# Kernel optimization log

Measured on AMD Instinct MI355X. Metric: run time of the kernel, lower is better.

Reference implementation:

```python
import jax, jax.numpy as jnp
import numpy as np

BITS = 4
N_PACK = 8          # 32-bit words / 4-bit values
GROUPSIZE = 128
MASK = (1 << BITS) - 1


def dequantize(qweight, qzeros, scales):
    """GPTQ/optimum-format int4 dequant.
    qweight: [in/8, out] int32, little-endian nibbles along packed (input) dim.
    qzeros:  [groups, out/8] int32, little-endian nibbles along packed (output) dim.
    scales:  [groups, out] float.
    Returns W: [in, out] float.
    """
    shifts = (jnp.arange(N_PACK, dtype=jnp.int32) * BITS)
    kpack, out_f = qweight.shape
    groups = scales.shape[0]
    # unpack weight nibbles -> [in, out]
    w_int = (qweight[:, None, :] >> shifts[None, :, None]) & MASK        # [in/8, 8, out]
    w_int = w_int.reshape(kpack * N_PACK, out_f)                          # [in, out]
    # unpack zero-point nibbles -> [groups, out]; optimum format adds 1 back
    zp = (qzeros[:, :, None] >> shifts[None, None, :]) & MASK             # [groups, out/8, 8]
    zp = zp.reshape(groups, out_f) + 1                                    # [groups, out]
    # group-wise dequant: (w - zp) * scale
    w_g = w_int.reshape(groups, GROUPSIZE, out_f).astype(scales.dtype)    # [G, gs, out]
    W = (w_g - zp[:, None, :].astype(scales.dtype)) * scales[:, None, :]
    return W.reshape(kpack * N_PACK, out_f)


def setup_inputs() -> dict:
    key = jax.random.key(0)
    k1, k2, k3, k4, k5 = jax.random.split(key, 5)
    in_f, out_f, groups = 4096, 11008, 4096 // GROUPSIZE
    tokens = 4096
    x = jax.random.normal(k1, (tokens, in_f), dtype=jnp.float32)
    qweight = jax.random.randint(k2, (in_f // N_PACK, out_f), 0, 2147483647, dtype=jnp.int32)
    qzeros = jax.random.randint(k3, (groups, out_f // N_PACK), 0, 2147483647, dtype=jnp.int32)
    scales = jax.random.uniform(k4, (groups, out_f), dtype=jnp.float32) * 0.01 + 0.001
    bias = jax.random.normal(k5, (out_f,), dtype=jnp.float32)
    return {"x": x, "qweight": qweight, "qzeros": qzeros, "scales": scales, "bias": bias}


def reference(x, qweight, qzeros, scales, bias):
    W = dequantize(qweight, qzeros, scales)   # [in, out]
    return x @ W + bias                        # F.linear(x, W.T, bias)
```

## Files before the change

### kernel.cpp

```cpp
#include <hip/hip_runtime.h>
#include <stdint.h>

typedef _Float16 h2 __attribute__((ext_vector_type(2)));
typedef _Float16 h8 __attribute__((ext_vector_type(8)));
typedef float f32x4 __attribute__((ext_vector_type(4)));

__device__ __forceinline__ uint32_t pk_cvt(float a, float b) {
  return __builtin_bit_cast(uint32_t, __builtin_amdgcn_cvt_pkrtz(a, b));
}

__device__ __forceinline__ uint32_t dq(uint32_t t, h2 z2, h2 s2) {
  h2 v = __builtin_bit_cast(h2, t);
  h2 w = (v - z2) * s2;
  return __builtin_bit_cast(uint32_t, w);
}

__device__ __forceinline__ uint32_t dq_lin(uint32_t u, h2 z2, h2 s2) {
  uint32_t t = (u & 0xFu) | ((u & 0xF0u) << 12) | 0x64006400u;
  return dq(t, z2, s2);
}

typedef __attribute__((address_space(1))) const uint32_t* gas_ptr;
typedef __attribute__((address_space(3))) uint32_t* las_ptr;
__device__ __forceinline__ void gll16(const _Float16* g, _Float16* l) {
  __builtin_amdgcn_global_load_lds((gas_ptr)g, (las_ptr)l, 16, 0, 0);
}

#define WAITVM(n) asm volatile("s_waitcnt vmcnt(" #n ")" ::: "memory")
#define MEMFENCE  asm volatile("" ::: "memory")

__global__ __launch_bounds__(256) void cvt_x_kernel(const float* __restrict__ x,
                                                    _Float16* __restrict__ xh,
                                                    size_t n) {
  size_t i = ((size_t)blockIdx.x * 256 + threadIdx.x) * 8;
  if (i >= n) return;
  float4 a = *(const float4*)(x + i);
  float4 b = *(const float4*)(x + i + 4);
  uint4 v = make_uint4(pk_cvt(a.x, a.y), pk_cvt(a.z, a.w),
                       pk_cvt(b.x, b.y), pk_cvt(b.z, b.w));
  *(uint4*)(xh + i) = v;
}

__global__ __launch_bounds__(256) void dequant_w_kernel(
    const uint32_t* __restrict__ qweight, const uint32_t* __restrict__ qzeros,
    const float* __restrict__ scales, _Float16* __restrict__ wt, int N, int K) {
  __shared__ uint32_t qw[8][64];
  const int t = threadIdx.x;
  const int n0 = blockIdx.x * 64;
  const int kp0 = blockIdx.y * 8;

  {
    int r = t >> 6, c = t & 63;
    qw[r][c]     = qweight[(size_t)(kp0 + r) * N + n0 + c];
    qw[r + 4][c] = qweight[(size_t)(kp0 + r + 4) * N + n0 + c];
  }
  __syncthreads();

  const int nl = t >> 2;
  const int kpl = (t & 3) * 2;
  const int n = n0 + nl;
  const int g = kp0 >> 4;
  uint32_t qz = qzeros[(size_t)g * (N >> 3) + (n >> 3)];
  int zp = (qz >> ((n & 7) * 4)) & 15;
  float sc = scales[(size_t)g * N + n];
  _Float16 hz = (_Float16)(float)(1024 + zp + 1);
  _Float16 hs = (_Float16)sc;
  h2 z2 = {hz, hz};
  h2 s2 = {hs, hs};

#pragma unroll
  for (int w = 0; w < 2; ++w) {
    uint32_t word = qw[kpl + w][nl];
    uint4 v = make_uint4(dq_lin(word, z2, s2), dq_lin(word >> 8, z2, s2),
                         dq_lin(word >> 16, z2, s2), dq_lin(word >> 24, z2, s2));
    *(uint4*)(wt + (size_t)n * K + (size_t)(kp0 + kpl + w) * 8) = v;
  }
}

__global__ __launch_bounds__(512, 2) void gemm_f16_256(
    const _Float16* __restrict__ A, const _Float16* __restrict__ B,
    const float* __restrict__ bias, float* __restrict__ out,
    int M, int N, int K) {
  __shared__ _Float16 As[4][256 * 32];
  __shared__ _Float16 Bs[4][256 * 32];

  const int gx = gridDim.x, gy = gridDim.y;
  const int nwg = gx * gy;
  const int lin = blockIdx.y * gx + blockIdx.x;
  const int xcd = lin & 7, idx = lin >> 3;
  const int q8 = nwg >> 3, r8 = nwg & 7;
  const int wg = (xcd < r8 ? xcd * (q8 + 1) : r8 * (q8 + 1) + (xcd - r8) * q8) + idx;
  const int bn0 = (wg % gx) * 256;
  const int bm0 = (wg / gx) * 256;

  const int tid = threadIdx.x;
  const int lane = tid & 63;
  const int wave = tid >> 6;
  const int wm = wave >> 2;
  const int wn = wave & 3;

  f32x4 acc[8][4];
#pragma unroll
  for (int i = 0; i < 8; ++i)
#pragma unroll
    for (int j = 0; j < 4; ++j) acc[i][j] = (f32x4)0.f;

  const int srow = lane >> 2;
  const int sslot = (lane & 3) ^ ((lane >> 3) & 3);
  const _Float16* pSa0 = A + (size_t)(bm0 + 32 * wave + srow) * K + sslot * 8;
  const _Float16* pSa1 = pSa0 + (size_t)16 * K;
  const _Float16* pSb0 = B + (size_t)(bn0 + 32 * wave + srow) * K + sslot * 8;
  const _Float16* pSb1 = pSb0 + (size_t)16 * K;
  const int dst_off = wave * 1024;

  const int fslot = ((lane >> 4) ^ ((lane >> 1) & 3)) * 8;
  const int aoff = (wm * 128 + (lane & 15)) * 32 + fslot;
  const int boff = (wn * 64 + (lane & 15)) * 32 + fslot;

  const int nt = K >> 5;

#pragma unroll
  for (int u = 0; u < 3; ++u) {
    if (u < nt) {
      const size_t ko = (size_t)u * 32;
      _Float16* da = As[u & 3] + dst_off;
      _Float16* db = Bs[u & 3] + dst_off;
      gll16(pSa0 + ko, da);
      gll16(pSa1 + ko, da + 512);
      gll16(pSb0 + ko, db);
      gll16(pSb1 + ko, db + 512);
    }
  }
  if (nt >= 3)      WAITVM(8);
  else if (nt == 2) WAITVM(4);
  else              WAITVM(0);
  __builtin_amdgcn_s_barrier();
  MEMFENCE;

  for (int t = 0; t < nt; ++t) {
    const int buf = t & 3;
    const _Float16* Ab = As[buf] + aoff;
    const _Float16* Bb = Bs[buf] + boff;
    const int ts = t + 3;
    const bool do_stage = ts < nt;
    const size_t ko = (size_t)ts * 32;
    _Float16* da = As[ts & 3] + dst_off;
    _Float16* db = Bs[ts & 3] + dst_off;

    h8 af[4], bf[4];
#pragma unroll
    for (int r = 0; r < 4; ++r) {
      af[r] = *(const h8*)(Ab + r * 512);
      bf[r] = *(const h8*)(Bb + r * 512);
    }
    if (do_stage) {
      gll16(pSa0 + ko, da);
      gll16(pSa1 + ko, da + 512);
    }
    __builtin_amdgcn_s_barrier();
    asm volatile("s_waitcnt lgkmcnt(0)" ::: "memory");
    __builtin_amdgcn_sched_barrier(0);
    __builtin_amdgcn_s_setprio(1);
#pragma unroll
    for (int r = 0; r < 4; ++r)
#pragma unroll
      for (int j = 0; j < 4; ++j)
        acc[r][j] = __builtin_amdgcn_mfma_f32_16x16x32_f16(af[r], bf[j],
                                                           acc[r][j], 0, 0, 0);
    __builtin_amdgcn_s_setprio(0);
    __builtin_amdgcn_s_barrier();
    MEMFENCE;

#pragma unroll
    for (int r = 0; r < 4; ++r) af[r] = *(const h8*)(Ab + (4 + r) * 512);
    if (do_stage) {
      gll16(pSb0 + ko, db);
      gll16(pSb1 + ko, db + 512);
    }
    if (do_stage)            WAITVM(8);
    else if (ts == nt)       WAITVM(4);
    else if (t + 2 == nt)    WAITVM(0);
    __builtin_amdgcn_s_barrier();
    asm volatile("s_waitcnt lgkmcnt(0)" ::: "memory");
    __builtin_amdgcn_sched_barrier(0);
    __builtin_amdgcn_s_setprio(1);
#pragma unroll
    for (int r = 0; r < 4; ++r)
#pragma unroll
      for (int j = 0; j < 4; ++j)
        acc[4 + r][j] = __builtin_amdgcn_mfma_f32_16x16x32_f16(af[r], bf[j],
                                                               acc[4 + r][j],
                                                               0, 0, 0);
    __builtin_amdgcn_s_setprio(0);
    __builtin_amdgcn_s_barrier();
    MEMFENCE;
  }

  const int r0 = bm0 + wm * 128 + ((lane >> 4) << 2);
  const int c0 = bn0 + wn * 64 + (lane & 15);
#pragma unroll
  for (int j = 0; j < 4; ++j) {
    const int c = c0 + j * 16;
    const float bv = bias[c];
#pragma unroll
    for (int i = 0; i < 8; ++i) {
#pragma unroll
      for (int rr = 0; rr < 4; ++rr)
        out[(size_t)(r0 + i * 16 + rr) * N + c] = acc[i][j][rr] + bv;
    }
  }
}

__global__ __launch_bounds__(256) void gemm_f16_kernel(
    const _Float16* __restrict__ A,
    const _Float16* __restrict__ B,
    const float* __restrict__ bias, float* __restrict__ out,
    int M, int N, int K) {
  __shared__ _Float16 As[128 * 32];
  __shared__ _Float16 Bs[128 * 32];

  const int tid = threadIdx.x;
  const int lane = tid & 63;
  const int wave = tid >> 6;
  const int wm = wave & 1;
  const int wn = wave >> 1;
  const int bn0 = blockIdx.x * 128;
  const int bm0 = blockIdx.y * 128;

  f32x4 acc[4][4];
#pragma unroll
  for (int i = 0; i < 4; ++i)
#pragma unroll
    for (int j = 0; j < 4; ++j) acc[i][j] = (f32x4)0.f;

  const int srow = wave * 16 + (lane >> 2);
  const int skoff = (lane & 3) * 8;
  const _Float16* Ag0 = A + (size_t)(bm0 + srow) * K + skoff;
  const _Float16* Ag1 = A + (size_t)(bm0 + 64 + srow) * K + skoff;
  const _Float16* Bg0 = B + (size_t)(bn0 + srow) * K + skoff;
  const _Float16* Bg1 = B + (size_t)(bn0 + 64 + srow) * K + skoff;
  _Float16* Al0 = As + (wave * 16) * 32;
  _Float16* Al1 = As + (64 + wave * 16) * 32;
  _Float16* Bl0 = Bs + (wave * 16) * 32;
  _Float16* Bl1 = Bs + (64 + wave * 16) * 32;

  const _Float16* Af = As + (wm * 64 + (lane & 15)) * 32 + (lane >> 4) * 8;
  const _Float16* Bf = Bs + (wn * 64 + (lane & 15)) * 32 + (lane >> 4) * 8;

  for (int k0 = 0; k0 < K; k0 += 32) {
    gll16(Ag0 + k0, Al0);
    gll16(Ag1 + k0, Al1);
    gll16(Bg0 + k0, Bl0);
    gll16(Bg1 + k0, Bl1);
    __syncthreads();

    h8 af[4], bf[4];
#pragma unroll
    for (int i = 0; i < 4; ++i) {
      af[i] = *(const h8*)(Af + i * 16 * 32);
      bf[i] = *(const h8*)(Bf + i * 16 * 32);
    }
#pragma unroll
    for (int i = 0; i < 4; ++i)
#pragma unroll
      for (int j = 0; j < 4; ++j)
        acc[i][j] = __builtin_amdgcn_mfma_f32_16x16x32_f16(af[i], bf[j],
                                                           acc[i][j], 0, 0, 0);
    __syncthreads();
  }

  const int r0 = bm0 + wm * 64 + (lane >> 4) * 4;
  const int c0 = bn0 + wn * 64 + (lane & 15);
#pragma unroll
  for (int j = 0; j < 4; ++j) {
    const int c = c0 + j * 16;
    const float bv = bias[c];
#pragma unroll
    for (int i = 0; i < 4; ++i) {
#pragma unroll
      for (int rr = 0; rr < 4; ++rr) {
        out[(size_t)(r0 + i * 16 + rr) * N + c] = acc[i][j][rr] + bv;
      }
    }
  }
}

#define LDK 40
__global__ __launch_bounds__(256) void gptq_gemm_fused(
    const float* __restrict__ x, const uint32_t* __restrict__ qweight,
    const uint32_t* __restrict__ qzeros, const float* __restrict__ scales,
    const float* __restrict__ bias, float* __restrict__ out,
    int M, int N, int K) {
  __shared__ _Float16 As[128 * LDK];
  __shared__ _Float16 Bs[128 * LDK];
  const int tid = threadIdx.x, lane = tid & 63, wave = tid >> 6;
  const int wm = wave & 1, wn = wave >> 1;
  const int bn0 = blockIdx.x * 128, bm0 = blockIdx.y * 128;
  const int sr = tid >> 1, sg0 = (tid & 1) * 2;
  const float* xrow = x + (size_t)(bm0 + sr) * K + sg0 * 8;
  const int colb = bn0 + sr;
  const int groups = K >> 7, NP = N >> 3;
  f32x4 acc[4][4];
#pragma unroll
  for (int i = 0; i < 4; ++i)
#pragma unroll
    for (int j = 0; j < 4; ++j) acc[i][j] = (f32x4)0.f;
  const _Float16* Ab = As + (wm * 64 + (lane & 15)) * LDK + (lane >> 4) * 8;
  const _Float16* Bb = Bs + (wn * 64 + (lane & 15)) * LDK + (lane >> 4) * 8;
  for (int g = 0; g < groups; ++g) {
    uint32_t qz = qzeros[(size_t)g * NP + (colb >> 3)];
    int zp = (qz >> ((colb & 7) * 4)) & 15;
    float sc = scales[(size_t)g * N + colb];
    _Float16 hz = (_Float16)(float)(1024 + zp + 1);
    _Float16 hs = (_Float16)sc;
    h2 z2 = {hz, hz}, s2 = {hs, hs};
#pragma unroll
    for (int kt = 0; kt < 4; ++kt) {
      const int k0 = g * 128 + kt * 32;
      const float* xr = xrow + k0;
      float4 fa0 = *(const float4*)(xr);
      float4 fa1 = *(const float4*)(xr + 4);
      float4 fa2 = *(const float4*)(xr + 8);
      float4 fa3 = *(const float4*)(xr + 12);
      const size_t kp = (size_t)(k0 >> 3) + sg0;
      uint32_t q0 = qweight[kp * N + colb];
      uint32_t q1 = qweight[(kp + 1) * N + colb];
      __syncthreads();
      uint4 av0 = make_uint4(pk_cvt(fa0.x, fa1.x), pk_cvt(fa0.y, fa1.y),
                             pk_cvt(fa0.z, fa1.z), pk_cvt(fa0.w, fa1.w));
      uint4 av1 = make_uint4(pk_cvt(fa2.x, fa3.x), pk_cvt(fa2.y, fa3.y),
                             pk_cvt(fa2.z, fa3.z), pk_cvt(fa2.w, fa3.w));
      *(uint4*)(As + sr * LDK + sg0 * 8) = av0;
      *(uint4*)(As + sr * LDK + sg0 * 8 + 8) = av1;
      uint4 bv0 = make_uint4(dq((q0 & 0x000F000Fu) | 0x64006400u, z2, s2),
                             dq(((q0 >> 4) & 0x000F000Fu) | 0x64006400u, z2, s2),
                             dq(((q0 >> 8) & 0x000F000Fu) | 0x64006400u, z2, s2),
                             dq(((q0 >> 12) & 0x000F000Fu) | 0x64006400u, z2, s2));
      uint4 bv1 = make_uint4(dq((q1 & 0x000F000Fu) | 0x64006400u, z2, s2),
                             dq(((q1 >> 4) & 0x000F000Fu) | 0x64006400u, z2, s2),
                             dq(((q1 >> 8) & 0x000F000Fu) | 0x64006400u, z2, s2),
                             dq(((q1 >> 12) & 0x000F000Fu) | 0x64006400u, z2, s2));
      *(uint4*)(Bs + sr * LDK + sg0 * 8) = bv0;
      *(uint4*)(Bs + sr * LDK + sg0 * 8 + 8) = bv1;
      __syncthreads();
      h8 af[4], bf[4];
#pragma unroll
      for (int i = 0; i < 4; ++i) {
        af[i] = *(const h8*)(Ab + i * 16 * LDK);
        bf[i] = *(const h8*)(Bb + i * 16 * LDK);
      }
#pragma unroll
      for (int i = 0; i < 4; ++i)
#pragma unroll
        for (int j = 0; j < 4; ++j)
          acc[i][j] = __builtin_amdgcn_mfma_f32_16x16x32_f16(af[i], bf[j],
                                                             acc[i][j], 0, 0, 0);
    }
  }
  const int r0 = bm0 + wm * 64 + (lane >> 4) * 4;
  const int c0 = bn0 + wn * 64 + (lane & 15);
#pragma unroll
  for (int j = 0; j < 4; ++j) {
    const int c = c0 + j * 16;
    const float bv = bias[c];
#pragma unroll
    for (int i = 0; i < 4; ++i)
#pragma unroll
      for (int rr = 0; rr < 4; ++rr)
        out[(size_t)(r0 + i * 16 + rr) * N + c] = acc[i][j][rr] + bv;
  }
}

extern "C" void kernel_launch(void* const* d_in, const int* in_sizes, int n_in,
                              void* d_out, int out_size, void* d_ws, size_t ws_size,
                              hipStream_t stream) {
  const float* x = (const float*)d_in[0];
  const uint32_t* qweight = (const uint32_t*)d_in[1];
  const uint32_t* qzeros = (const uint32_t*)d_in[2];
  const float* scales = (const float*)d_in[3];
  const float* bias = (const float*)d_in[4];
  float* out = (float*)d_out;

  const int out_f = in_sizes[4];
  const int groups = in_sizes[3] / out_f;
  const int in_f = groups * 128;
  const int tokens = in_sizes[0] / in_f;

  const size_t need = ((size_t)tokens * in_f + (size_t)out_f * in_f) * 2;
  if (ws_size >= need) {
    _Float16* xh = (_Float16*)d_ws;
    _Float16* wt = xh + (size_t)tokens * in_f;

    size_t nx = (size_t)tokens * in_f;
    cvt_x_kernel<<<(nx + 2047) / 2048, 256, 0, stream>>>(x, xh, nx);

    dim3 gq(out_f / 64, (in_f / 8) / 8);
    dequant_w_kernel<<<gq, 256, 0, stream>>>(qweight, qzeros, scales, wt,
                                             out_f, in_f);

    if ((tokens % 256) == 0 && (out_f % 256) == 0 && (in_f % 32) == 0) {
      dim3 gg(out_f / 256, tokens / 256);
      gemm_f16_256<<<gg, 512, 0, stream>>>(xh, wt, bias, out,
                                           tokens, out_f, in_f);
    } else {
      dim3 gg(out_f / 128, tokens / 128);
      gemm_f16_kernel<<<gg, 256, 0, stream>>>(xh, wt, bias, out,
                                              tokens, out_f, in_f);
    }
  } else {
    dim3 grid(out_f / 128, tokens / 128);
    gptq_gemm_fused<<<grid, 256, 0, stream>>>(x, qweight, qzeros, scales, bias,
                                              out, tokens, out_f, in_f);
  }
}
```

Measured before the change: 656.0 us.

## Merge prep kernels and cut GEMM main-loop barriers to one per iteration

Fuses the x fp32→fp16 conversion and the weight dequant into one launch, splitting work by a flat block index, which removes one kernel launch. In the 256-tile GEMM, each K step now has a single wait-and-barrier at the top instead of four barriers. Each step loads all A and B fragments up front, issues all four global→LDS stage loads together, and uses lgkmcnt waits to overlap the LDS reads with the first MFMA half. The cost is more live fragment registers, and the reordered waits depend on vmcnt accounting across the 4-buffer ring staying correct.

```diff
diff --git a/kernel.cpp b/kernel.cpp
--- a/kernel.cpp
+++ b/kernel.cpp
@@ -27,27 +27,31 @@
 }
 
 #define WAITVM(n) asm volatile("s_waitcnt vmcnt(" #n ")" ::: "memory")
+#define WAITLGKM(n) asm volatile("s_waitcnt lgkmcnt(" #n ")" ::: "memory")
 #define MEMFENCE  asm volatile("" ::: "memory")
 
-__global__ __launch_bounds__(256) void cvt_x_kernel(const float* __restrict__ x,
-                                                    _Float16* __restrict__ xh,
-                                                    size_t n) {
-  size_t i = ((size_t)blockIdx.x * 256 + threadIdx.x) * 8;
-  if (i >= n) return;
-  float4 a = *(const float4*)(x + i);
-  float4 b = *(const float4*)(x + i + 4);
-  uint4 v = make_uint4(pk_cvt(a.x, a.y), pk_cvt(a.z, a.w),
-                       pk_cvt(b.x, b.y), pk_cvt(b.z, b.w));
-  *(uint4*)(xh + i) = v;
-}
-
-__global__ __launch_bounds__(256) void dequant_w_kernel(
+__global__ __launch_bounds__(256) void prep_kernel(
+    const float* __restrict__ x, _Float16* __restrict__ xh, size_t nx,
+    int nxb,
     const uint32_t* __restrict__ qweight, const uint32_t* __restrict__ qzeros,
     const float* __restrict__ scales, _Float16* __restrict__ wt, int N, int K) {
   __shared__ uint32_t qw[8][64];
+  const int bid = blockIdx.x;
+  if (bid < nxb) {
+    size_t i = ((size_t)bid * 256 + threadIdx.x) * 8;
+    if (i >= nx) return;
+    float4 a = *(const float4*)(x + i);
+    float4 b = *(const float4*)(x + i + 4);
+    uint4 v = make_uint4(pk_cvt(a.x, a.y), pk_cvt(a.z, a.w),
+                         pk_cvt(b.x, b.y), pk_cvt(b.z, b.w));
+    *(uint4*)(xh + i) = v;
+    return;
+  }
+  const int dqb = bid - nxb;
+  const int nblk = N >> 6;
   const int t = threadIdx.x;
-  const int n0 = blockIdx.x * 64;
-  const int kp0 = blockIdx.y * 8;
+  const int n0 = (dqb % nblk) * 64;
+  const int kp0 = (dqb / nblk) * 8;
 
   {
     int r = t >> 6, c = t & 63;
@@ -131,69 +135,59 @@
       gll16(pSb1 + ko, db + 512);
     }
   }
-  if (nt >= 3)      WAITVM(8);
-  else if (nt == 2) WAITVM(4);
-  else              WAITVM(0);
-  __builtin_amdgcn_s_barrier();
-  MEMFENCE;
 
   for (int t = 0; t < nt; ++t) {
+    if (t < nt - 2)       WAITVM(8);
+    else if (t == nt - 2) WAITVM(4);
+    else                  WAITVM(0);
+    __builtin_amdgcn_s_barrier();
+    MEMFENCE;
+
     const int buf = t & 3;
     const _Float16* Ab = As[buf] + aoff;
     const _Float16* Bb = Bs[buf] + boff;
+
+    h8 bf[4], af0[4], af1[4];
+#pragma unroll
+    for (int r = 0; r < 4; ++r) bf[r] = *(const h8*)(Bb + r * 512);
+#pragma unroll
+    for (int r = 0; r < 4; ++r) af0[r] = *(const h8*)(Ab + r * 512);
+#pragma unroll
+    for (int r = 0; r < 4; ++r) af1[r] = *(const h8*)(Ab + (4 + r) * 512);
+
     const int ts = t + 3;
-    const bool do_stage = ts < nt;
-    const size_t ko = (size_t)ts * 32;
-    _Float16* da = As[ts & 3] + dst_off;
-    _Float16* db = Bs[ts & 3] + dst_off;
-
-    h8 af[4], bf[4];
-#pragma unroll
-    for (int r = 0; r < 4; ++r) {
-      af[r] = *(const h8*)(Ab + r * 512);
-      bf[r] = *(const h8*)(Bb + r * 512);
-    }
-    if (do_stage) {
+    if (ts < nt) {
+      const size_t ko = (size_t)ts * 32;
+      _Float16* da = As[ts & 3] + dst_off;
+      _Float16* db = Bs[ts & 3] + dst_off;
       gll16(pSa0 + ko, da);
       gll16(pSa1 + ko, da + 512);
-    }
-    __builtin_amdgcn_s_barrier();
-    asm volatile("s_waitcnt lgkmcnt(0)" ::: "memory");
+      gll16(pSb0 + ko, db);
+      gll16(pSb1 + ko, db + 512);
+    }
+
+    WAITLGKM(4);
     __builtin_amdgcn_sched_barrier(0);
     __builtin_amdgcn_s_setprio(1);
 #pragma unroll
     for (int r = 0; r < 4; ++r)
 #pragma unroll
       for (int j = 0; j < 4; ++j)
-        acc[r][j] = __builtin_amdgcn_mfma_f32_16x16x32_f16(af[r], bf[j],
+        acc[r][j] = __builtin_amdgcn_mfma_f32_16x16x32_f16(af0[r], bf[j],
                                                            acc[r][j], 0, 0, 0);
     __builtin_amdgcn_s_setprio(0);
-    __builtin_amdgcn_s_barrier();
-    MEMFENCE;
-
-#pragma unroll
-    for (int r = 0; r < 4; ++r) af[r] = *(const h8*)(Ab + (4 + r) * 512);
-    if (do_stage) {
-      gll16(pSb0 + ko, db);
-      gll16(pSb1 + ko, db + 512);
-    }
-    if (do_stage)            WAITVM(8);
-    else if (ts == nt)       WAITVM(4);
-    else if (t + 2 == nt)    WAITVM(0);
-    __builtin_amdgcn_s_barrier();
-    asm volatile("s_waitcnt lgkmcnt(0)" ::: "memory");
+
+    WAITLGKM(0);
     __builtin_amdgcn_sched_barrier(0);
     __builtin_amdgcn_s_setprio(1);
 #pragma unroll
     for (int r = 0; r < 4; ++r)
 #pragma unroll
       for (int j = 0; j < 4; ++j)
-        acc[4 + r][j] = __builtin_amdgcn_mfma_f32_16x16x32_f16(af[r], bf[j],
+        acc[4 + r][j] = __builtin_amdgcn_mfma_f32_16x16x32_f16(af1[r], bf[j],
                                                                acc[4 + r][j],
                                                                0, 0, 0);
     __builtin_amdgcn_s_setprio(0);
-    __builtin_amdgcn_s_barrier();
-    MEMFENCE;
   }
 
   const int r0 = bm0 + wm * 128 + ((lane >> 4) << 2);
@@ -392,11 +386,10 @@
     _Float16* wt = xh + (size_t)tokens * in_f;
 
     size_t nx = (size_t)tokens * in_f;
-    cvt_x_kernel<<<(nx + 2047) / 2048, 256, 0, stream>>>(x, xh, nx);
-
-    dim3 gq(out_f / 64, (in_f / 8) / 8);
-    dequant_w_kernel<<<gq, 256, 0, stream>>>(qweight, qzeros, scales, wt,
-                                             out_f, in_f);
+    const int nxb = (int)((nx + 2047) / 2048);
+    const int ndq = (out_f / 64) * (in_f / 64);
+    prep_kernel<<<nxb + ndq, 256, 0, stream>>>(x, xh, nx, nxb, qweight, qzeros,
+                                               scales, wt, out_f, in_f);
 
     if ((tokens % 256) == 0 && (out_f % 256) == 0 && (in_f % 32) == 0) {
       dim3 gg(out_f / 256, tokens / 256);
```

Measured after the change: 607.3 us. 7.4% less time.
